# Kernel optimization log

Measured on AMD Instinct MI355X. Metric: run time of the kernel, lower is better.

## Reference

```python
import jax, jax.numpy as jnp
import numpy as np

B, S, D = 4, 1024, 1024
NS = 8            # n_samples
NT = 10           # n_steps
EXP_NOISE = 0.1
STEP = 0.01
TEMP = 1.0
LN_EPS = 1e-5


def _ln(x, g, b):
    m = jnp.mean(x, axis=-1, keepdims=True)
    v = jnp.mean(jnp.square(x - m), axis=-1, keepdims=True)
    return (x - m) * jax.lax.rsqrt(v + LN_EPS) * g + b


def setup_inputs() -> dict:
    key = jax.random.key(0)
    ks = jax.random.split(key, 8)
    sc = 0.02
    return {
        "hidden": jax.random.normal(ks[0], (B, S, D), jnp.float32),
        "W1": jax.random.normal(ks[1], (D, 2 * D), jnp.float32) * sc,
        "b1": jnp.zeros((2 * D,), jnp.float32),
        "ln1_g": jnp.ones((2 * D,), jnp.float32),
        "ln1_b": jnp.zeros((2 * D,), jnp.float32),
        "W2": jax.random.normal(ks[2], (2 * D, D), jnp.float32) * sc,
        "b2": jnp.zeros((D,), jnp.float32),
        "Ew1": jax.random.normal(ks[3], (2 * D, D), jnp.float32) * sc,
        "Eb1": jnp.zeros((D,), jnp.float32),
        "Eln_g": jnp.ones((D,), jnp.float32),
        "Eln_b": jnp.zeros((D,), jnp.float32),
        "Ew2": jax.random.normal(ks[4], (D, D // 2), jnp.float32) * sc,
        "Eb2": jnp.zeros((D // 2,), jnp.float32),
        "Ew3": jax.random.normal(ks[5], (D // 2, 1), jnp.float32) * sc,
        "Eb3": jnp.zeros((1,), jnp.float32),
    }


def reference(hidden, W1, b1, ln1_g, ln1_b, W2, b2,
              Ew1, Eb1, Eln_g, Eln_b, Ew2, Eb2, Ew3, Eb3):
    # context: per-seq mean, identical at every position (keepdim+expand in torch)
    ctx = jnp.mean(hidden, axis=1)                      # [B, D]
    # context_predictor (result is .detach()-ed inside pcn_refine)
    cp = jax.nn.relu(_ln(ctx @ W1 + b1, ln1_g, ln1_b)) @ W2 + b2   # [B, D]
    cp = jax.lax.stop_gradient(cp)

    nkey = jax.random.key(42)
    # n_samples exploration hypotheses: hidden + N(0, exploration_noise)
    expl = jax.random.normal(jax.random.fold_in(nkey, 0), (NS, B, S, D), hidden.dtype)
    hyp = hidden[None] + expl * EXP_NOISE               # [NS, B, S, D]

    cpb = cp[None, :, None, :]                          # broadcast to [NS,B,S,D]

    # PCN refinement: linear pull toward cp + small noise on all but last step
    def step_fn(cur, t):
        cur = cur - STEP * (cur - cpb)
        noise = jax.random.normal(jax.random.fold_in(nkey, t + 1), cur.shape, cur.dtype)
        cur = cur + noise * 0.01 * (t < NT - 1)
        return cur, None

    hyp, _ = jax.lax.scan(step_fn, hyp, jnp.arange(NT))

    # energy_net on concat([latent, context]): split first linear to avoid concat
    Ew1_h, Ew1_c = Ew1[:D], Ew1[D:]
    ce = ctx @ Ew1_c + Eb1                              # context contribution [B, D]
    e = hyp @ Ew1_h + ce[None, :, None, :]              # [NS, B, S, D]
    e = jax.nn.relu(_ln(e, Eln_g, Eln_b))
    e = jax.nn.relu(e @ Ew2 + Eb2)                      # [NS, B, S, D//2]
    e = (e @ Ew3 + Eb3)[..., 0]                         # [NS, B, S]
    energies = jnp.mean(e, axis=2)                      # [NS, B]

    probs = jax.nn.softmax(-energies / TEMP, axis=0)    # [NS, B]
    selected = jnp.einsum('nb,nbsd->bsd', probs, hyp)   # [B, S, D]
    return selected
```

## Files before the change

kernel.cpp:

```cpp
#include <hip/hip_runtime.h>
#include <hip/hip_bf16.h>
#include <stdint.h>
#include <math.h>


#define NS_ 8
#define B_ 4
#define S_ 1024
#define D_ 1024
#define NROWS (NS_*B_*S_)
#define NELEM (1u<<25)

typedef __attribute__((ext_vector_type(8))) short short8;
typedef __attribute__((ext_vector_type(4))) float f32x4;

struct RngParams {
  uint32_t k0[10], k1[10];
  float coef[10];
  float aH, aCP;
};

__host__ __device__ __forceinline__ uint32_t rotl32_(uint32_t x, int r) {
#if defined(__HIP_DEVICE_COMPILE__)
  return __builtin_rotateleft32(x, (uint32_t)r);
#else
  return (x << r) | (x >> (32 - r));
#endif
}

__host__ __device__ __forceinline__ void tf2x32(uint32_t k0, uint32_t k1,
                                                uint32_t x0, uint32_t x1,
                                                uint32_t &o0, uint32_t &o1) {
  uint32_t k2 = k0 ^ k1 ^ 0x1BD11BDAu;
  x0 += k0; x1 += k1;
  x0 += x1; x1 = rotl32_(x1, 13); x1 ^= x0;
  x0 += x1; x1 = rotl32_(x1, 15); x1 ^= x0;
  x0 += x1; x1 = rotl32_(x1, 26); x1 ^= x0;
  x0 += x1; x1 = rotl32_(x1, 6);  x1 ^= x0;
  x0 += k1; x1 += k2 + 1u;
  x0 += x1; x1 = rotl32_(x1, 17); x1 ^= x0;
  x0 += x1; x1 = rotl32_(x1, 29); x1 ^= x0;
  x0 += x1; x1 = rotl32_(x1, 16); x1 ^= x0;
  x0 += x1; x1 = rotl32_(x1, 24); x1 ^= x0;
  x0 += k2; x1 += k0 + 2u;
  x0 += x1; x1 = rotl32_(x1, 13); x1 ^= x0;
  x0 += x1; x1 = rotl32_(x1, 15); x1 ^= x0;
  x0 += x1; x1 = rotl32_(x1, 26); x1 ^= x0;
  x0 += x1; x1 = rotl32_(x1, 6);  x1 ^= x0;
  x0 += k0; x1 += k1 + 3u;
  x0 += x1; x1 = rotl32_(x1, 17); x1 ^= x0;
  x0 += x1; x1 = rotl32_(x1, 29); x1 ^= x0;
  x0 += x1; x1 = rotl32_(x1, 16); x1 ^= x0;
  x0 += x1; x1 = rotl32_(x1, 24); x1 ^= x0;
  x0 += k1; x1 += k2 + 4u;
  x0 += x1; x1 = rotl32_(x1, 13); x1 ^= x0;
  x0 += x1; x1 = rotl32_(x1, 15); x1 ^= x0;
  x0 += x1; x1 = rotl32_(x1, 26); x1 ^= x0;
  x0 += x1; x1 = rotl32_(x1, 6);  x1 ^= x0;
  x0 += k2; x1 += k0 + 5u;
  o0 = x0; o1 = x1;
}

__device__ __forceinline__ float b2n_scaled(uint32_t bits) {
  const float lo = -0.99999994f;
  float f = __uint_as_float((bits >> 9) | 0x3f800000u);
  float x = fmaxf(lo, fmaf(f, 2.0f, lo - 2.0f));
  float t = fmaf(-x, x, 1.0f);
  float l2 = __log2f(t);
  float p;
  if (l2 > -7.2134752f) {
    float v = fmaf(l2, -1.0f, -3.6067376f);
    p = 2.11766e-09f;
    p = fmaf(p, v, 3.73196e-08f);
    p = fmaf(p, v, -5.52622e-07f);
    p = fmaf(p, v, -9.93683e-07f);
    p = fmaf(p, v, 7.13556e-05f);
    p = fmaf(p, v, -5.90466e-04f);
    p = fmaf(p, v, -2.83857e-03f);
    p = fmaf(p, v, 2.41772e-01f);
    p = fmaf(p, v, 2.1233136f);
  } else {
    float s = sqrtf(l2 * -0.69314718f) - 3.0f;
    p = -2.83146e-04f;
    p = fmaf(p, s, 1.42766e-04f);
    p = fmaf(p, s, 1.90826e-03f);
    p = fmaf(p, s, -5.19503e-03f);
    p = fmaf(p, s, 8.11695e-03f);
    p = fmaf(p, s, -1.07799e-02f);
    p = fmaf(p, s, 1.33486e-02f);
    p = fmaf(p, s, 1.41658104f);
    p = fmaf(p, s, 4.00643763f);
  }
  return p * x;
}

__device__ __forceinline__ void noise10x2(const RngParams& P, uint32_t i0,
                                          float& n0, float& n1) {
  float a0 = 0.f, a1 = 0.f;
  #pragma unroll 2
  for (int j = 0; j < 10; ++j) {
    uint32_t w0, w1, v0, v1;
    tf2x32(P.k0[j], P.k1[j], 0u, i0, w0, w1);
    tf2x32(P.k0[j], P.k1[j], 0u, i0 + 1u, v0, v1);
    float c = P.coef[j];
    a0 = fmaf(c, b2n_scaled(w0 ^ w1), a0);
    a1 = fmaf(c, b2n_scaled(v0 ^ v1), a1);
  }
  n0 = a0; n1 = a1;
}

__device__ __forceinline__ float noise10(const RngParams& P, uint32_t i) {
  float acc = 0.f;
  #pragma unroll 2
  for (int j = 0; j < 10; ++j) {
    uint32_t w0, w1;
    tf2x32(P.k0[j], P.k1[j], 0u, i, w0, w1);
    acc = fmaf(P.coef[j], b2n_scaled(w0 ^ w1), acc);
  }
  return acc;
}

__device__ __forceinline__ uint16_t bf16u(float x) {
  __hip_bfloat16 h = __float2bfloat16(x);
  return *(uint16_t*)&h;
}
__device__ __forceinline__ float bf2f(uint32_t u) {
  return __uint_as_float(u << 16);
}

__device__ void wcvt_body(const float* __restrict__ src, uint16_t* __restrict__ dst,
                          int K, int N, int bx, int by) {
  __shared__ float tile[64][65];
  int n0 = bx * 64, k0 = by * 64;
  int tid = threadIdx.x;
  #pragma unroll
  for (int i = 0; i < 16; ++i) {
    int lin = tid + i * 256;
    int tr = lin >> 6, tc = lin & 63;
    tile[tr][tc] = src[(size_t)(k0 + tr) * N + n0 + tc];
  }
  __syncthreads();
  #pragma unroll
  for (int i = 0; i < 8; ++i) {
    int lin = tid + i * 256;
    int tr = lin >> 5, tc2 = (lin & 31) * 2;
    uint32_t pk = (uint32_t)bf16u(tile[tc2][tr]) | ((uint32_t)bf16u(tile[tc2 + 1][tr]) << 16);
    *(uint32_t*)(&dst[(size_t)(n0 + tr) * K + k0 + tc2]) = pk;
  }
}

__global__ void k_prep(const float* __restrict__ Ew1, const float* __restrict__ Ew2,
                       const float* __restrict__ hidden,
                       uint16_t* __restrict__ WT1, uint16_t* __restrict__ WT2,
                       float* __restrict__ part) {
  int bi = blockIdx.x;
  if (bi < 256) {
    wcvt_body(Ew1, WT1, 1024, 1024, bi & 15, bi >> 4);
  } else if (bi < 384) {
    int j = bi - 256;
    wcvt_body(Ew2, WT2, 1024, 512, j & 7, j >> 3);
  } else {
    int cb = bi - 384;
    int b = cb >> 6, ch = cb & 63;
    const float* p = hidden + (size_t)b * (S_ * D_) + (size_t)ch * 16 * 1024;
    int tid = threadIdx.x;
    #pragma unroll
    for (int k = 0; k < 4; ++k) {
      int d = tid + k * 256;
      float s = 0.f;
      #pragma unroll
      for (int t = 0; t < 16; ++t) s += p[t * 1024 + d];
      part[(size_t)cb * 1024 + d] = s;
    }
  }
}

__global__ void k_ctxB(const float* __restrict__ part, float* __restrict__ ctx) {
  int idx = blockIdx.x * 256 + threadIdx.x;
  int b = idx >> 10, d = idx & 1023;
  float s = 0.f;
  #pragma unroll 8
  for (int c = 0; c < 64; ++c) s += part[((size_t)(b * 64 + c)) * 1024 + d];
  ctx[idx] = s * (1.0f / 1024.0f);
}

__global__ void k_fc1(const float* __restrict__ ctx, const float* __restrict__ W1,
                      const float* __restrict__ b1, float* __restrict__ t1) {
  __shared__ float red[4][64];
  int b = blockIdx.x >> 5;
  int j0 = (blockIdx.x & 31) * 64;
  int l = threadIdx.x & 63, w = threadIdx.x >> 6;
  int j = j0 + l;
  const float* c = ctx + b * 1024 + w * 256;
  const float* wp = W1 + (size_t)(w * 256) * 2048 + j;
  float s = 0.f;
  #pragma unroll 8
  for (int k = 0; k < 256; ++k) s += c[k] * wp[(size_t)k * 2048];
  red[w][l] = s; __syncthreads();
  if (w == 0)
    t1[b * 2048 + j] = red[0][l] + red[1][l] + red[2][l] + red[3][l] + b1[j];
}

__global__ void k_ln_relu(float* __restrict__ t1, const float* __restrict__ g,
                          const float* __restrict__ bb) {
  __shared__ float red[256];
  int row = blockIdx.x, tid = threadIdx.x;
  float* x = t1 + row * 2048;
  float v[8];
  #pragma unroll
  for (int q = 0; q < 8; ++q) v[q] = x[tid + q * 256];
  float s = 0.f;
  #pragma unroll
  for (int q = 0; q < 8; ++q) s += v[q];
  red[tid] = s; __syncthreads();
  for (int off = 128; off > 0; off >>= 1) { if (tid < off) red[tid] += red[tid + off]; __syncthreads(); }
  float m = red[0] * (1.0f / 2048.0f);
  __syncthreads();
  float s2 = 0.f;
  #pragma unroll
  for (int q = 0; q < 8; ++q) { float d = v[q] - m; s2 += d * d; }
  red[tid] = s2; __syncthreads();
  for (int off = 128; off > 0; off >>= 1) { if (tid < off) red[tid] += red[tid + off]; __syncthreads(); }
  float var = red[0] * (1.0f / 2048.0f);
  float rs = 1.0f / sqrtf(var + 1e-5f);
  #pragma unroll
  for (int q = 0; q < 8; ++q) {
    int j = tid + q * 256;
    float z = (v[q] - m) * rs * g[j] + bb[j];
    x[j] = fmaxf(z, 0.0f);
  }
}

__global__ void k_fc2(const float* __restrict__ t1, const float* __restrict__ W2,
                      const float* __restrict__ b2, const float* __restrict__ ctx,
                      const float* __restrict__ Ew1c, const float* __restrict__ Eb1,
                      float* __restrict__ cp, float* __restrict__ ce) {
  __shared__ float red[4][64];
  int b = blockIdx.x >> 4;
  int j0 = (blockIdx.x & 15) * 64;
  int l = threadIdx.x & 63, w = threadIdx.x >> 6;
  int j = j0 + l;
  float s = 0.f;
  if (blockIdx.y == 0) {
    const float* a = t1 + b * 2048 + w * 512;
    const float* wp = W2 + (size_t)(w * 512) * 1024 + j;
    #pragma unroll 8
    for (int k = 0; k < 512; ++k) s += a[k] * wp[(size_t)k * 1024];
  } else {
    const float* a = ctx + b * 1024 + w * 256;
    const float* wp = Ew1c + (size_t)(w * 256) * 1024 + j;
    #pragma unroll 8
    for (int k = 0; k < 256; ++k) s += a[k] * wp[(size_t)k * 1024];
  }
  red[w][l] = s; __syncthreads();
  if (w == 0) {
    float r = red[0][l] + red[1][l] + red[2][l] + red[3][l];
    if (blockIdx.y == 0) cp[b * 1024 + j] = r + b2[j];
    else                 ce[b * 1024 + j] = r + Eb1[j];
  }
}

#define ZP_OF   0
#define APAN_OF 32768

__device__ __forceinline__ int pswz(int row, int byteInRow) {
  return (row * 2048 + byteInRow) ^ ((row & 7) << 4);
}

template<bool BIG>
__global__ __launch_bounds__(256, BIG ? 5 : 2) void k_fused(
    const float* __restrict__ hidden, const float* __restrict__ cp,
    const float* __restrict__ ce, uint32_t* __restrict__ hypPairs,
    const uint16_t* __restrict__ WT1, const uint16_t* __restrict__ WT2,
    const float* __restrict__ Eln_g, const float* __restrict__ Eln_b,
    const float* __restrict__ Eb2, const float* __restrict__ Ew3,
    float* __restrict__ erows, float* __restrict__ bscr, RngParams P)
{
  __shared__ __align__(16) char smem[BIG ? 32768 : 65536];
  const int tid = threadIdx.x;
  const int lane = tid & 63;
  const int w = tid >> 6;
  const int rl = lane & 15;
  const int kg = lane >> 4;
  const int r0 = blockIdx.x * 16;
  const int bidx = (r0 >> 10) & 3;
  float* bs = bscr + (size_t)blockIdx.x * 256;

  const float2* cp2 = (const float2*)(cp + (bidx << 10));
  const float2 cvA = cp2[tid];
  const float2 cvB = cp2[tid + 256];
  #pragma unroll 1
  for (int q = 0; q < 32; ++q) {
    int p = tid + q * 256;
    int row = p >> 9, c0 = (p & 511) * 2;
    uint32_t i0 = (uint32_t)(r0 + row) * 1024u + (uint32_t)c0;
    float nz0, nz1;
    noise10x2(P, i0, nz0, nz1);
    float2 hv = *(const float2*)(hidden + (i0 & 0x3FFFFFu));
    float2 cv = (q & 1) ? cvB : cvA;
    float h0 = fmaf(P.aH, hv.x, fmaf(P.aCP, cv.x, nz0));
    float h1 = fmaf(P.aH, hv.y, fmaf(P.aCP, cv.y, nz1));
    uint32_t pk = (uint32_t)bf16u(h0) | ((uint32_t)bf16u(h1) << 16);
    if (BIG) hypPairs[i0 >> 1] = pk;
    else *(uint32_t*)(smem + APAN_OF + pswz(row, c0 * 2)) = pk;
  }
  __syncthreads();

  float s1a[4] = {0.f, 0.f, 0.f, 0.f};
  float s2a[4] = {0.f, 0.f, 0.f, 0.f};
  const uint16_t* Abase = (const uint16_t*)hypPairs + (size_t)(r0 + rl) * 1024 + kg * 8;
  for (int g = 0; g < 4; ++g) {
    f32x4 acc[4] = {};
    const uint16_t* b0 = WT1 + (size_t)(g * 256 + w * 64 +  0 + rl) * 1024 + kg * 8;
    const uint16_t* b1p = WT1 + (size_t)(g * 256 + w * 64 + 16 + rl) * 1024 + kg * 8;
    const uint16_t* b2p = WT1 + (size_t)(g * 256 + w * 64 + 32 + rl) * 1024 + kg * 8;
    const uint16_t* b3p = WT1 + (size_t)(g * 256 + w * 64 + 48 + rl) * 1024 + kg * 8;
    #pragma unroll 8
    for (int kt = 0; kt < 32; ++kt) {
      short8 af;
      if (BIG) af = *(const short8*)(Abase + kt * 32);
      else     af = *(const short8*)(smem + APAN_OF + pswz(rl, kt * 64 + kg * 16));
      short8 f0 = *(const short8*)(b0  + kt * 32);
      short8 f1 = *(const short8*)(b1p + kt * 32);
      short8 f2 = *(const short8*)(b2p + kt * 32);
      short8 f3 = *(const short8*)(b3p + kt * 32);
      acc[0] = __builtin_amdgcn_mfma_f32_16x16x32_bf16(af, f0, acc[0], 0, 0, 0);
      acc[1] = __builtin_amdgcn_mfma_f32_16x16x32_bf16(af, f1, acc[1], 0, 0, 0);
      acc[2] = __builtin_amdgcn_mfma_f32_16x16x32_bf16(af, f2, acc[2], 0, 0, 0);
      acc[3] = __builtin_amdgcn_mfma_f32_16x16x32_bf16(af, f3, acc[3], 0, 0, 0);
    }
    #pragma unroll
    for (int j = 0; j < 4; ++j) {
      int C = g * 256 + w * 64 + j * 16 + rl;
      float cev = ce[(bidx << 10) + C];
      #pragma unroll
      for (int i = 0; i < 4; ++i) {
        float y = acc[j][i] + cev;
        s1a[i] += y;
        s2a[i] = fmaf(y, y, s2a[i]);
        *(uint16_t*)(smem + ZP_OF + pswz(kg * 4 + i, C * 2)) = bf16u(y);
      }
    }
  }
  #pragma unroll
  for (int i = 0; i < 4; ++i) {
    #pragma unroll
    for (int m = 1; m < 16; m <<= 1) {
      s1a[i] += __shfl_xor(s1a[i], m);
      s2a[i] += __shfl_xor(s2a[i], m);
    }
  }
  if (rl == 0) {
    #pragma unroll
    for (int i = 0; i < 4; ++i) {
      bs[(w * 16 + kg * 4 + i) * 2 + 0] = s1a[i];
      bs[(w * 16 + kg * 4 + i) * 2 + 1] = s2a[i];
    }
  }
  __syncthreads();

  if (tid < 16) {
    float s1 = 0.f, s2 = 0.f;
    #pragma unroll
    for (int wv = 0; wv < 4; ++wv) {
      s1 += bs[(wv * 16 + tid) * 2 + 0];
      s2 += bs[(wv * 16 + tid) * 2 + 1];
    }
    float m = s1 * (1.0f / 1024.0f);
    float var = fmaxf(s2 * (1.0f / 1024.0f) - m * m, 0.0f);
    bs[128 + tid] = m;
    bs[144 + tid] = 1.0f / sqrtf(var + 1e-5f);
  }
  __syncthreads();

  {
    float gv[4], bv[4];
    #pragma unroll
    for (int qq = 0; qq < 4; ++qq) {
      gv[qq] = Eln_g[tid + qq * 256];
      bv[qq] = Eln_b[tid + qq * 256];
    }
    #pragma unroll 1
    for (int row = 0; row < 16; ++row) {
      float m = bs[128 + row], rs = bs[144 + row];
      #pragma unroll
      for (int qq = 0; qq < 4; ++qq) {
        int col = tid + qq * 256;
        uint16_t* zp = (uint16_t*)(smem + ZP_OF + pswz(row, col * 2));
        float v = bf2f(*zp);
        float z = fmaf((v - m) * rs, gv[qq], bv[qq]);
        *zp = bf16u(fmaxf(z, 0.f));
      }
    }
  }
  __syncthreads();

  float ep0 = 0.f, ep1 = 0.f, ep2 = 0.f, ep3 = 0.f;
  for (int g = 0; g < 2; ++g) {
    f32x4 acc[4] = {};
    const uint16_t* b0 = WT2 + (size_t)(g * 256 + w * 64 +  0 + rl) * 1024 + kg * 8;
    const uint16_t* b1p = WT2 + (size_t)(g * 256 + w * 64 + 16 + rl) * 1024 + kg * 8;
    const uint16_t* b2p = WT2 + (size_t)(g * 256 + w * 64 + 32 + rl) * 1024 + kg * 8;
    const uint16_t* b3p = WT2 + (size_t)(g * 256 + w * 64 + 48 + rl) * 1024 + kg * 8;
    #pragma unroll 8
    for (int kt = 0; kt < 32; ++kt) {
      short8 af = *(const short8*)(smem + ZP_OF + pswz(rl, kt * 64 + kg * 16));
      short8 f0 = *(const short8*)(b0  + kt * 32);
      short8 f1 = *(const short8*)(b1p + kt * 32);
      short8 f2 = *(const short8*)(b2p + kt * 32);
      short8 f3 = *(const short8*)(b3p + kt * 32);
      acc[0] = __builtin_amdgcn_mfma_f32_16x16x32_bf16(af, f0, acc[0], 0, 0, 0);
      acc[1] = __builtin_amdgcn_mfma_f32_16x16x32_bf16(af, f1, acc[1], 0, 0, 0);
      acc[2] = __builtin_amdgcn_mfma_f32_16x16x32_bf16(af, f2, acc[2], 0, 0, 0);
      acc[3] = __builtin_amdgcn_mfma_f32_16x16x32_bf16(af, f3, acc[3], 0, 0, 0);
    }
    #pragma unroll
    for (int j = 0; j < 4; ++j) {
      int C = g * 256 + w * 64 + j * 16 + rl;
      float eb = Eb2[C], w3 = Ew3[C];
      ep0 = fmaf(fmaxf(acc[j][0] + eb, 0.f), w3, ep0);
      ep1 = fmaf(fmaxf(acc[j][1] + eb, 0.f), w3, ep1);
      ep2 = fmaf(fmaxf(acc[j][2] + eb, 0.f), w3, ep2);
      ep3 = fmaf(fmaxf(acc[j][3] + eb, 0.f), w3, ep3);
    }
  }
  #pragma unroll
  for (int m = 1; m < 16; m <<= 1) {
    ep0 += __shfl_xor(ep0, m);
    ep1 += __shfl_xor(ep1, m);
    ep2 += __shfl_xor(ep2, m);
    ep3 += __shfl_xor(ep3, m);
  }
  if (rl == 0) {
    bs[192 + w * 16 + kg * 4 + 0] = ep0;
    bs[192 + w * 16 + kg * 4 + 1] = ep1;
    bs[192 + w * 16 + kg * 4 + 2] = ep2;
    bs[192 + w * 16 + kg * 4 + 3] = ep3;
  }
  __syncthreads();
  if (tid < 16)
    erows[r0 + tid] = bs[192 + tid] + bs[208 + tid] + bs[224 + tid] + bs[240 + tid];
}

__global__ void k_energy(const float* __restrict__ erows, const float* __restrict__ Eb3,
                         float* __restrict__ energ) {
  __shared__ float red[256];
  int nb = blockIdx.x, tid = threadIdx.x;
  const float* x = erows + nb * 1024;
  float s = x[tid] + x[tid + 256] + x[tid + 512] + x[tid + 768];
  red[tid] = s; __syncthreads();
  for (int off = 128; off > 0; off >>= 1) { if (tid < off) red[tid] += red[tid + off]; __syncthreads(); }
  if (tid == 0) energ[nb] = red[0] * (1.0f / 1024.0f) + Eb3[0];
}

template<bool BIG>
__global__ __launch_bounds__(256) void k_select(
    const float* __restrict__ hidden, const float* __restrict__ cp,
    const float* __restrict__ energ, const uint32_t* __restrict__ hypPairs,
    float* __restrict__ out, RngParams P)
{
  uint32_t pe = blockIdx.x * 256u + threadIdx.x;
  uint32_t i0 = pe * 2u;
  uint32_t b = (i0 >> 20) & 3u;
  float e[8];
  #pragma unroll
  for (int n = 0; n < 8; ++n) e[n] = -energ[n * 4 + b];
  float mx = e[0];
  #pragma unroll
  for (int n = 1; n < 8; ++n) mx = fmaxf(mx, e[n]);
  float p[8]; float s = 0.f;
  #pragma unroll
  for (int n = 0; n < 8; ++n) { p[n] = expf(e[n] - mx); s += p[n]; }
  float inv = 1.0f / s;
  float a0 = 0.f, a1 = 0.f;
  if (BIG) {
    #pragma unroll
    for (int n = 0; n < 8; ++n) {
      uint32_t pk = hypPairs[pe + ((uint32_t)n << 21)];
      a0 = fmaf(p[n], __uint_as_float(pk << 16), a0);
      a1 = fmaf(p[n], __uint_as_float(pk & 0xffff0000u), a1);
    }
    *(float2*)(out + i0) = make_float2(a0 * inv, a1 * inv);
  } else {
    float2 hv = *(const float2*)(hidden + i0);
    float2 cv = *(const float2*)(cp + ((b << 10) | (i0 & 1023u)));
    #pragma unroll
    for (int n = 0; n < 8; ++n) {
      a0 = fmaf(p[n], noise10(P, i0 + ((uint32_t)n << 22)), a0);
      a1 = fmaf(p[n], noise10(P, i0 + 1u + ((uint32_t)n << 22)), a1);
    }
    float o0 = fmaf(P.aH, hv.x, P.aCP * cv.x) + a0 * inv;
    float o1 = fmaf(P.aH, hv.y, P.aCP * cv.y) + a1 * inv;
    *(float2*)(out + i0) = make_float2(o0, o1);
  }
}

extern "C" void kernel_launch(void* const* d_in, const int* in_sizes, int n_in,
                              void* d_out, int out_size, void* d_ws, size_t ws_size,
                              hipStream_t stream) {
  const float* hidden = (const float*)d_in[0];
  const float* W1    = (const float*)d_in[1];
  const float* b1    = (const float*)d_in[2];
  const float* ln1_g = (const float*)d_in[3];
  const float* ln1_b = (const float*)d_in[4];
  const float* W2    = (const float*)d_in[5];
  const float* b2    = (const float*)d_in[6];
  const float* Ew1   = (const float*)d_in[7];
  const float* Eb1   = (const float*)d_in[8];
  const float* Eln_g = (const float*)d_in[9];
  const float* Eln_b = (const float*)d_in[10];
  const float* Ew2   = (const float*)d_in[11];
  const float* Eb2   = (const float*)d_in[12];
  const float* Ew3   = (const float*)d_in[13];
  const float* Eb3   = (const float*)d_in[14];
  float* out = (float*)d_out;

  const size_t HYP_B  = (size_t)NELEM * 2;
  const size_t WT1_B  = 1024ull * 1024 * 2;
  const size_t WT2_B  = 512ull * 1024 * 2;
  const size_t PART_B = 256ull * 1024 * 4;
  const size_t BSCR_B = 2048ull * 256 * 4;
  const size_t SMALL_B = (4096 + 8192 + 4096 + 4096 + 32768 + 32) * 4;
  bool big = ws_size >= HYP_B + WT1_B + WT2_B + PART_B + BSCR_B + SMALL_B + 1024;

  char* ws = (char*)d_ws;
  uint32_t* hypPairs = nullptr;
  size_t off = 0;
  if (big) { hypPairs = (uint32_t*)ws; off += HYP_B; }
  uint16_t* WT1 = (uint16_t*)(ws + off); off += WT1_B;
  uint16_t* WT2 = (uint16_t*)(ws + off); off += WT2_B;
  float* part  = (float*)(ws + off);     off += PART_B;
  float* bscr  = (float*)(ws + off);     off += BSCR_B;
  float* ctx   = (float*)(ws + off);
  float* t1    = ctx + 4096;
  float* cp    = t1 + 8192;
  float* ce    = cp + 4096;
  float* erows = ce + 4096;
  float* energ = erows + 32768;

  RngParams P;
  for (uint32_t t = 0; t < 10; ++t) {
    uint32_t o0, o1;
    tf2x32(0u, 42u, 0u, t, o0, o1);
    P.k0[t] = o0; P.k1[t] = o1;
  }
  double a = pow(0.99, 10);
  P.coef[0] = (float)(0.1 * a);
  for (int j = 1; j <= 9; ++j) P.coef[j] = (float)(0.01 * pow(0.99, 10 - j));
  P.aH = (float)a;
  P.aCP = (float)(1.0 - a);

  k_prep<<<640, 256, 0, stream>>>(Ew1, Ew2, hidden, WT1, WT2, part);
  k_ctxB<<<16, 256, 0, stream>>>(part, ctx);
  k_fc1<<<128, 256, 0, stream>>>(ctx, W1, b1, t1);
  k_ln_relu<<<4, 256, 0, stream>>>(t1, ln1_g, ln1_b);
  k_fc2<<<dim3(64, 2), 256, 0, stream>>>(t1, W2, b2, ctx, Ew1 + (size_t)1024 * 1024, Eb1, cp, ce);
  if (big)
    k_fused<true><<<2048, 256, 0, stream>>>(hidden, cp, ce, hypPairs, WT1, WT2,
                                            Eln_g, Eln_b, Eb2, Ew3, erows, bscr, P);
  else
    k_fused<false><<<2048, 256, 0, stream>>>(hidden, cp, ce, (uint32_t*)ws, WT1, WT2,
                                             Eln_g, Eln_b, Eb2, Ew3, erows, bscr, P);
  k_energy<<<32, 256, 0, stream>>>(erows, Eb3, energ);
  if (big)
    k_select<true><<<8192, 256, 0, stream>>>(hidden, cp, energ, hypPairs, out, P);
  else
    k_select<false><<<8192, 256, 0, stream>>>(hidden, cp, energ, nullptr, out, P);
}
```

Measured before the change: 1.073 ms.

## Run second energy GEMM in FP8 and move block scratch into LDS

Converts Ew2 to FP8 e4m3 and stores the post-LN activations as FP8 in LDS, switching the second GEMM to fp8 MFMA. This halves the LDS footprint, which lets the launch bound rise from 5 to 8 blocks per CU. It also moves the per-block reduction scratch from global memory into shared memory. FP8 quantization of the activations and weights lowers accuracy of the energies, which risks changing the softmax selection weights.

```diff
diff --git a/kernel.cpp b/kernel.cpp
--- a/kernel.cpp
+++ b/kernel.cpp
@@ -1,5 +1,6 @@
 #include <hip/hip_runtime.h>
 #include <hip/hip_bf16.h>
+#include <hip/hip_fp8.h>
 #include <stdint.h>
 #include <math.h>
 
@@ -13,6 +14,7 @@
 
 typedef __attribute__((ext_vector_type(8))) short short8;
 typedef __attribute__((ext_vector_type(4))) float f32x4;
+typedef long i64;
 
 struct RngParams {
   uint32_t k0[10], k1[10];
@@ -127,6 +129,15 @@
 __device__ __forceinline__ float bf2f(uint32_t u) {
   return __uint_as_float(u << 16);
 }
+__device__ __forceinline__ uint8_t f2e4m3(float x) {
+  __hip_fp8_e4m3 h(x);
+  return (uint8_t)h.__x;
+}
+__device__ __forceinline__ float e4m32f(uint8_t u) {
+  __hip_fp8_e4m3 h;
+  h.__x = u;
+  return (float)h;
+}
 
 __device__ void wcvt_body(const float* __restrict__ src, uint16_t* __restrict__ dst,
                           int K, int N, int bx, int by) {
@@ -149,16 +160,37 @@
   }
 }
 
+__device__ void wcvt8_body(const float* __restrict__ src, uint8_t* __restrict__ dst,
+                           int K, int N, int bx, int by) {
+  __shared__ float tile[64][65];
+  int n0 = bx * 64, k0 = by * 64;
+  int tid = threadIdx.x;
+  #pragma unroll
+  for (int i = 0; i < 16; ++i) {
+    int lin = tid + i * 256;
+    int tr = lin >> 6, tc = lin & 63;
+    tile[tr][tc] = src[(size_t)(k0 + tr) * N + n0 + tc];
+  }
+  __syncthreads();
+  #pragma unroll
+  for (int i = 0; i < 8; ++i) {
+    int lin = tid + i * 256;
+    int tr = lin >> 5, tc2 = (lin & 31) * 2;
+    uint16_t pk = (uint16_t)f2e4m3(tile[tc2][tr]) | ((uint16_t)f2e4m3(tile[tc2 + 1][tr]) << 8);
+    *(uint16_t*)(&dst[(size_t)(n0 + tr) * K + k0 + tc2]) = pk;
+  }
+}
+
 __global__ void k_prep(const float* __restrict__ Ew1, const float* __restrict__ Ew2,
                        const float* __restrict__ hidden,
-                       uint16_t* __restrict__ WT1, uint16_t* __restrict__ WT2,
+                       uint16_t* __restrict__ WT1, uint8_t* __restrict__ WT2,
                        float* __restrict__ part) {
   int bi = blockIdx.x;
   if (bi < 256) {
     wcvt_body(Ew1, WT1, 1024, 1024, bi & 15, bi >> 4);
   } else if (bi < 384) {
     int j = bi - 256;
-    wcvt_body(Ew2, WT2, 1024, 512, j & 7, j >> 3);
+    wcvt8_body(Ew2, WT2, 1024, 512, j & 7, j >> 3);
   } else {
     int cb = bi - 384;
     int b = cb >> 6, ch = cb & 63;
@@ -260,23 +292,31 @@
   }
 }
 
-#define ZP_OF   0
-#define APAN_OF 32768
+#define ZP_OF    0
+#define RED2_OF  16384
+#define STM_OF   16896
+#define STR_OF   16960
+#define RED_OF   17024
+#define SMEM_END 17280
+#define APAN_OF  17280
 
 __device__ __forceinline__ int pswz(int row, int byteInRow) {
   return (row * 2048 + byteInRow) ^ ((row & 7) << 4);
 }
+__device__ __forceinline__ int pswz8(int row, int byteInRow) {
+  return (row * 1024 + (byteInRow ^ ((row & 7) << 3)));
+}
 
 template<bool BIG>
-__global__ __launch_bounds__(256, BIG ? 5 : 2) void k_fused(
+__global__ __launch_bounds__(256, BIG ? 8 : 2) void k_fused(
     const float* __restrict__ hidden, const float* __restrict__ cp,
     const float* __restrict__ ce, uint32_t* __restrict__ hypPairs,
-    const uint16_t* __restrict__ WT1, const uint16_t* __restrict__ WT2,
+    const uint16_t* __restrict__ WT1, const uint8_t* __restrict__ WT2,
     const float* __restrict__ Eln_g, const float* __restrict__ Eln_b,
     const float* __restrict__ Eb2, const float* __restrict__ Ew3,
-    float* __restrict__ erows, float* __restrict__ bscr, RngParams P)
+    float* __restrict__ erows, RngParams P)
 {
-  __shared__ __align__(16) char smem[BIG ? 32768 : 65536];
+  __shared__ __align__(16) char smem[BIG ? SMEM_END : (SMEM_END + 32768)];
   const int tid = threadIdx.x;
   const int lane = tid & 63;
   const int w = tid >> 6;
@@ -284,7 +324,10 @@
   const int kg = lane >> 4;
   const int r0 = blockIdx.x * 16;
   const int bidx = (r0 >> 10) & 3;
-  float* bs = bscr + (size_t)blockIdx.x * 256;
+  float* rowm = (float*)(smem + STM_OF);
+  float* rowr = (float*)(smem + STR_OF);
+  float* red  = (float*)(smem + RED_OF);
+  float* red2 = (float*)(smem + RED2_OF);
 
   const float2* cp2 = (const float2*)(cp + (bidx << 10));
   const float2 cvA = cp2[tid];
@@ -338,7 +381,7 @@
         float y = acc[j][i] + cev;
         s1a[i] += y;
         s2a[i] = fmaf(y, y, s2a[i]);
-        *(uint16_t*)(smem + ZP_OF + pswz(kg * 4 + i, C * 2)) = bf16u(y);
+        *(uint8_t*)(smem + ZP_OF + pswz8(kg * 4 + i, C)) = f2e4m3(y);
       }
     }
   }
@@ -353,8 +396,8 @@
   if (rl == 0) {
     #pragma unroll
     for (int i = 0; i < 4; ++i) {
-      bs[(w * 16 + kg * 4 + i) * 2 + 0] = s1a[i];
-      bs[(w * 16 + kg * 4 + i) * 2 + 1] = s2a[i];
+      red2[(w * 16 + kg * 4 + i) * 2 + 0] = s1a[i];
+      red2[(w * 16 + kg * 4 + i) * 2 + 1] = s2a[i];
     }
   }
   __syncthreads();
@@ -363,13 +406,13 @@
     float s1 = 0.f, s2 = 0.f;
     #pragma unroll
     for (int wv = 0; wv < 4; ++wv) {
-      s1 += bs[(wv * 16 + tid) * 2 + 0];
-      s2 += bs[(wv * 16 + tid) * 2 + 1];
+      s1 += red2[(wv * 16 + tid) * 2 + 0];
+      s2 += red2[(wv * 16 + tid) * 2 + 1];
     }
     float m = s1 * (1.0f / 1024.0f);
     float var = fmaxf(s2 * (1.0f / 1024.0f) - m * m, 0.0f);
-    bs[128 + tid] = m;
-    bs[144 + tid] = 1.0f / sqrtf(var + 1e-5f);
+    rowm[tid] = m;
+    rowr[tid] = 1.0f / sqrtf(var + 1e-5f);
   }
   __syncthreads();
 
@@ -382,14 +425,14 @@
     }
     #pragma unroll 1
     for (int row = 0; row < 16; ++row) {
-      float m = bs[128 + row], rs = bs[144 + row];
+      float m = rowm[row], rs = rowr[row];
       #pragma unroll
       for (int qq = 0; qq < 4; ++qq) {
         int col = tid + qq * 256;
-        uint16_t* zp = (uint16_t*)(smem + ZP_OF + pswz(row, col * 2));
-        float v = bf2f(*zp);
+        uint8_t* zp = (uint8_t*)(smem + ZP_OF + pswz8(row, col));
+        float v = e4m32f(*zp);
         float z = fmaf((v - m) * rs, gv[qq], bv[qq]);
-        *zp = bf16u(fmaxf(z, 0.f));
+        *zp = f2e4m3(fmaxf(z, 0.f));
       }
     }
   }
@@ -398,21 +441,21 @@
   float ep0 = 0.f, ep1 = 0.f, ep2 = 0.f, ep3 = 0.f;
   for (int g = 0; g < 2; ++g) {
     f32x4 acc[4] = {};
-    const uint16_t* b0 = WT2 + (size_t)(g * 256 + w * 64 +  0 + rl) * 1024 + kg * 8;
-    const uint16_t* b1p = WT2 + (size_t)(g * 256 + w * 64 + 16 + rl) * 1024 + kg * 8;
-    const uint16_t* b2p = WT2 + (size_t)(g * 256 + w * 64 + 32 + rl) * 1024 + kg * 8;
-    const uint16_t* b3p = WT2 + (size_t)(g * 256 + w * 64 + 48 + rl) * 1024 + kg * 8;
+    const uint8_t* b0 = WT2 + (size_t)(g * 256 + w * 64 +  0 + rl) * 1024 + kg * 8;
+    const uint8_t* b1p = WT2 + (size_t)(g * 256 + w * 64 + 16 + rl) * 1024 + kg * 8;
+    const uint8_t* b2p = WT2 + (size_t)(g * 256 + w * 64 + 32 + rl) * 1024 + kg * 8;
+    const uint8_t* b3p = WT2 + (size_t)(g * 256 + w * 64 + 48 + rl) * 1024 + kg * 8;
     #pragma unroll 8
     for (int kt = 0; kt < 32; ++kt) {
-      short8 af = *(const short8*)(smem + ZP_OF + pswz(rl, kt * 64 + kg * 16));
-      short8 f0 = *(const short8*)(b0  + kt * 32);
-      short8 f1 = *(const short8*)(b1p + kt * 32);
-      short8 f2 = *(const short8*)(b2p + kt * 32);
-      short8 f3 = *(const short8*)(b3p + kt * 32);
-      acc[0] = __builtin_amdgcn_mfma_f32_16x16x32_bf16(af, f0, acc[0], 0, 0, 0);
-      acc[1] = __builtin_amdgcn_mfma_f32_16x16x32_bf16(af, f1, acc[1], 0, 0, 0);
-      acc[2] = __builtin_amdgcn_mfma_f32_16x16x32_bf16(af, f2, acc[2], 0, 0, 0);
-      acc[3] = __builtin_amdgcn_mfma_f32_16x16x32_bf16(af, f3, acc[3], 0, 0, 0);
+      i64 af = *(const i64*)(smem + ZP_OF + pswz8(rl, kt * 32 + kg * 8));
+      i64 f0 = *(const i64*)(b0  + kt * 32);
+      i64 f1 = *(const i64*)(b1p + kt * 32);
+      i64 f2 = *(const i64*)(b2p + kt * 32);
+      i64 f3 = *(const i64*)(b3p + kt * 32);
+      acc[0] = __builtin_amdgcn_mfma_f32_16x16x32_fp8_fp8(af, f0, acc[0], 0, 0, 0);
+      acc[1] = __builtin_amdgcn_mfma_f32_16x16x32_fp8_fp8(af, f1, acc[1], 0, 0, 0);
+      acc[2] = __builtin_amdgcn_mfma_f32_16x16x32_fp8_fp8(af, f2, acc[2], 0, 0, 0);
+      acc[3] = __builtin_amdgcn_mfma_f32_16x16x32_fp8_fp8(af, f3, acc[3], 0, 0, 0);
     }
     #pragma unroll
     for (int j = 0; j < 4; ++j) {
@@ -432,14 +475,14 @@
     ep3 += __shfl_xor(ep3, m);
   }
   if (rl == 0) {
-    bs[192 + w * 16 + kg * 4 + 0] = ep0;
-    bs[192 + w * 16 + kg * 4 + 1] = ep1;
-    bs[192 + w * 16 + kg * 4 + 2] = ep2;
-    bs[192 + w * 16 + kg * 4 + 3] = ep3;
+    red[w * 16 + kg * 4 + 0] = ep0;
+    red[w * 16 + kg * 4 + 1] = ep1;
+    red[w * 16 + kg * 4 + 2] = ep2;
+    red[w * 16 + kg * 4 + 3] = ep3;
   }
   __syncthreads();
   if (tid < 16)
-    erows[r0 + tid] = bs[192 + tid] + bs[208 + tid] + bs[224 + tid] + bs[240 + tid];
+    erows[r0 + tid] = red[tid] + red[16 + tid] + red[32 + tid] + red[48 + tid];
 }
 
 __global__ void k_energy(const float* __restrict__ erows, const float* __restrict__ Eb3,
@@ -517,20 +560,18 @@
 
   const size_t HYP_B  = (size_t)NELEM * 2;
   const size_t WT1_B  = 1024ull * 1024 * 2;
-  const size_t WT2_B  = 512ull * 1024 * 2;
+  const size_t WT2_B  = 512ull * 1024;
   const size_t PART_B = 256ull * 1024 * 4;
-  const size_t BSCR_B = 2048ull * 256 * 4;
   const size_t SMALL_B = (4096 + 8192 + 4096 + 4096 + 32768 + 32) * 4;
-  bool big = ws_size >= HYP_B + WT1_B + WT2_B + PART_B + BSCR_B + SMALL_B + 1024;
+  bool big = ws_size >= HYP_B + WT1_B + WT2_B + PART_B + SMALL_B + 1024;
 
   char* ws = (char*)d_ws;
   uint32_t* hypPairs = nullptr;
   size_t off = 0;
   if (big) { hypPairs = (uint32_t*)ws; off += HYP_B; }
   uint16_t* WT1 = (uint16_t*)(ws + off); off += WT1_B;
-  uint16_t* WT2 = (uint16_t*)(ws + off); off += WT2_B;
+  uint8_t*  WT2 = (uint8_t*)(ws + off);  off += WT2_B;
   float* part  = (float*)(ws + off);     off += PART_B;
-  float* bscr  = (float*)(ws + off);     off += BSCR_B;
   float* ctx   = (float*)(ws + off);
   float* t1    = ctx + 4096;
   float* cp    = t1 + 8192;
@@ -557,10 +598,10 @@
   k_fc2<<<dim3(64, 2), 256, 0, stream>>>(t1, W2, b2, ctx, Ew1 + (size_t)1024 * 1024, Eb1, cp, ce);
   if (big)
     k_fused<true><<<2048, 256, 0, stream>>>(hidden, cp, ce, hypPairs, WT1, WT2,
-                                            Eln_g, Eln_b, Eb2, Ew3, erows, bscr, P);
+                                            Eln_g, Eln_b, Eb2, Ew3, erows, P);
   else
     k_fused<false><<<2048, 256, 0, stream>>>(hidden, cp, ce, (uint32_t*)ws, WT1, WT2,
-                                             Eln_g, Eln_b, Eb2, Ew3, erows, bscr, P);
+                                             Eln_g, Eln_b, Eb2, Ew3, erows, P);
   k_energy<<<32, 256, 0, stream>>>(erows, Eb3, energ);
   if (big)
     k_select<true><<<8192, 256, 0, stream>>>(hidden, cp, energ, hypPairs, out, P);
```

Result: no change. 1.072 ms (-0.1%).
